# Optimization experiments

Measured on AMD Instinct MI355X. Metric: run time of the kernel, lower is better.

## Reference

```python
import jax, jax.numpy as jnp
import numpy as np

DILATIONS = [1, 2, 4]


def _lstm_cell(x, h, c, W_ih, W_hh, b_ih, b_hh):
    # PyTorch LSTMCell: gates in i, f, g, o order
    gates = x @ W_ih.T + b_ih + h @ W_hh.T + b_hh
    i, f, g, o = jnp.split(gates, 4, axis=-1)
    c_new = jax.nn.sigmoid(f) * c + jax.nn.sigmoid(i) * jnp.tanh(g)
    h_new = jax.nn.sigmoid(o) * jnp.tanh(c_new)
    return h_new, c_new


def _drnn_forward(x, params):
    B, T, _ = x.shape
    H = params[0][1].shape[1]
    L = len(params)
    # static per-(t, layer) update mask from dilations
    masks = jnp.asarray(
        np.array([[t % d == 0 for d in DILATIONS] for t in range(T)], dtype=bool)
    )  # [T, L]

    hs0 = tuple(jnp.zeros((B, H), x.dtype) for _ in range(L))
    cs0 = tuple(jnp.zeros((B, H), x.dtype) for _ in range(L))

    def step(carry, inp):
        hs, cs = carry
        x_t, m = inp  # x_t: [B, F], m: [L] bool
        hs = list(hs)
        cs = list(cs)
        for l, (Wi, Wh, bi, bh) in enumerate(params):
            inp_l = x_t if l == 0 else hs[l - 1]
            h_new, c_new = _lstm_cell(inp_l, hs[l], cs[l], Wi, Wh, bi, bh)
            hs[l] = jnp.where(m[l], h_new, hs[l])
            cs[l] = jnp.where(m[l], c_new, cs[l])
        return (tuple(hs), tuple(cs)), hs[-1]

    _, ys = jax.lax.scan(step, (hs0, cs0), (jnp.swapaxes(x, 0, 1), masks))
    return jnp.swapaxes(ys, 0, 1)  # [B, T, H]


def setup_inputs() -> dict:
    key = jax.random.key(0)
    ks = jax.random.split(key, 16)
    B, T, F, H = 128, 1024, 128, 256
    k = 1.0 / np.sqrt(H)  # torch LSTMCell init scale

    def u(kk, shape):
        return jax.random.uniform(kk, shape, jnp.float32, -k, k)

    inp = {"x": jax.random.normal(ks[0], (B, T, F), jnp.float32)}
    in_sizes = [F, H, H]
    ki = 1
    for l in range(3):
        inp[f"W_ih{l}"] = u(ks[ki], (4 * H, in_sizes[l])); ki += 1
        inp[f"W_hh{l}"] = u(ks[ki], (4 * H, H)); ki += 1
        inp[f"b_ih{l}"] = u(ks[ki], (4 * H,)); ki += 1
        inp[f"b_hh{l}"] = u(ks[ki], (4 * H,)); ki += 1
    return inp


def reference(x, W_ih0, W_hh0, b_ih0, b_hh0,
              W_ih1, W_hh1, b_ih1, b_hh1,
              W_ih2, W_hh2, b_ih2, b_hh2):
    params = [
        (W_ih0, W_hh0, b_ih0, b_hh0),
        (W_ih1, W_hh1, b_ih1, b_hh1),
        (W_ih2, W_hh2, b_ih2, b_hh2),
    ]
    return _drnn_forward(x, params)
```

## Files before the change

### kernel.cpp

```cpp
#include <hip/hip_runtime.h>
#include <hip/hip_fp16.h>
#include <stdint.h>
#include <stddef.h>


typedef _Float16 f16;
typedef _Float16 v2h __attribute__((ext_vector_type(2)));
typedef _Float16 v8h __attribute__((ext_vector_type(8)));
typedef __fp16 h2_raw __attribute__((ext_vector_type(2)));
typedef __fp16 h8_raw __attribute__((ext_vector_type(8)));
typedef float v4f __attribute__((ext_vector_type(4)));
typedef unsigned long long u64;

#define DEVINL static __device__ __forceinline__

DEVINL float sigm(float x) { return 1.0f / (1.0f + __expf(-x)); }
DEVINL float tanh_(float x) {
  x = fminf(fmaxf(x, -15.0f), 15.0f);
  float e = __expf(-2.0f * x);
  return (1.0f - e) / (1.0f + e);
}
DEVINL v2h pack2(float a, float b) {
  return __builtin_bit_cast(v2h, __builtin_amdgcn_cvt_pkrtz(a, b));
}
DEVINL v4f mfma_16x16x32(v8h a, v8h b, v4f c) {
  return __builtin_amdgcn_mfma_f32_16x16x32_f16(__builtin_bit_cast(h8_raw, a),
                                                __builtin_bit_cast(h8_raw, b), c,
                                                0, 0, 0);
}


__global__ void k_cvt_x(const float2* __restrict__ src, v2h* __restrict__ dst, int n2) {
  int i = blockIdx.x * blockDim.x + threadIdx.x;
  int st = gridDim.x * blockDim.x;
  for (; i < n2; i += st) {
    float2 v = src[i];
    dst[i] = pack2(v.x, v.y);
  }
}

__global__ void k_prep_w(const float* __restrict__ wih0, const float* __restrict__ whh0,
                         const float* __restrict__ wih1, const float* __restrict__ whh1,
                         const float* __restrict__ wih2, const float* __restrict__ whh2,
                         const float* __restrict__ bi0, const float* __restrict__ bh0,
                         const float* __restrict__ bi1, const float* __restrict__ bh1,
                         const float* __restrict__ bi2, const float* __restrict__ bh2,
                         f16* wih0f, f16* whh0f, f16* wih1f, f16* whh1f,
                         f16* wih2f, f16* whh2f,
                         float* bias0, float* bias1, float* bias2) {
  int i = blockIdx.x * blockDim.x + threadIdx.x;
  if (i < 131072) wih0f[i] = (f16)wih0[i];
  whh0f[i] = (f16)whh0[i];
  wih1f[i] = (f16)wih1[i];
  whh1f[i] = (f16)whh1[i];
  wih2f[i] = (f16)wih2[i];
  whh2f[i] = (f16)whh2[i];
  if (i < 1024) {
    bias0[i] = bi0[i] + bh0[i];
    bias1[i] = bi1[i] + bh1[i];
    bias2[i] = bi2[i] + bh2[i];
  }
}


template <int K>
__launch_bounds__(256)
__global__ void k_gemm(const f16* __restrict__ A, int Tb, int t0,
                       const f16* __restrict__ W, const float* __restrict__ bias,
                       f16* __restrict__ G) {
  constexpr int LDK = K + 8;
  __shared__ f16 As[64 * LDK];
  int b = blockIdx.x >> 2, tb = blockIdx.x & 3;
  const f16* Ablk = A + ((size_t)b * Tb + t0 + tb * 64) * K;
  int tid = threadIdx.x;

  constexpr int NV = 64 * K / 8;
  const uint4* src = (const uint4*)Ablk;
  for (int i = tid; i < NV; i += 256) {
    int e = i * 8;
    int r = e / K, c0 = e % K;
    *(uint4*)&As[r * LDK + c0] = src[i];
  }
  __syncthreads();

  int wave = tid >> 6, lane = tid & 63;
  int lm = lane & 15, lk = (lane >> 4) * 8;

  v8h af[K / 32];
#pragma unroll
  for (int kc = 0; kc < K / 32; ++kc)
    af[kc] = *(const v8h*)&As[(wave * 16 + lm) * LDK + kc * 32 + lk];

  size_t grow0 = (size_t)b * 256 + tb * 64 + wave * 16;
  for (int nt = 0; nt < 64; ++nt) {
    v4f acc = {0.0f, 0.0f, 0.0f, 0.0f};
    const f16* Wrow = W + (size_t)(nt * 16 + lm) * K + lk;
#pragma unroll
    for (int kc = 0; kc < K / 32; ++kc) {
      v8h bf = *(const v8h*)(Wrow + kc * 32);
      acc = mfma_16x16x32(af[kc], bf, acc);
    }
    float bv = bias[nt * 16 + lm];
#pragma unroll
    for (int r = 0; r < 4; ++r) {
      int m = (lane >> 4) * 4 + r;
      G[(grow0 + m) * 1024 + nt * 16 + lm] = (f16)(acc[r] + bv);
    }
  }
}


template <int LAYER>
__launch_bounds__(512, 2)
__global__ void k_rec(const f16* __restrict__ G,
                      const f16* __restrict__ Whh,
                      int t0, int steps,
                      f16* __restrict__ Hout, float* __restrict__ y,
                      float* __restrict__ hstate, float* __restrict__ cstate,
                      u64* hxw) {
  int blk = blockIdx.x;
  int g = blk & 15, half = blk >> 4;
  int tid = threadIdx.x;
  int lane = tid & 63;
  int wv = tid >> 6;

  int q = wv & 3, cs = wv >> 2;
  int colbase = q * 256 + half * 128 + cs * 64;
  int arow = lane & 15;
  int kq = (lane >> 4) * 8;

  int bl = wv, p = lane;
  int b = g * 8 + bl;

  __shared__ __align__(16) f16 hbuf[16][264];
  __shared__ float gq[4][8][132];

  v8h wf[32];
#pragma unroll
  for (int nt = 0; nt < 4; ++nt)
#pragma unroll
    for (int kt = 0; kt < 8; ++kt)
      wf[nt * 8 + kt] =
          *(const v8h*)&Whh[(size_t)(colbase + nt * 16 + arow) * 256 + kt * 32 + kq];

  {
    uint32_t* hz = (uint32_t*)&hbuf[0][0];
    for (int i = tid; i < 16 * 264 / 2; i += 512) hz[i] = 0u;
  }
  __syncthreads();

  float c0 = 0.0f, c1 = 0.0f, h0f = 0.0f, h1f = 0.0f;
  if (t0 > 0) {
    for (int w = tid; w < 1024; w += 512) {
      int rb = w >> 7, kp = w & 127;
      float2 hv = *(const float2*)&hstate[(size_t)(g * 8 + rb) * 256 + 2 * kp];
      *(uint32_t*)&hbuf[rb][2 * kp] = __builtin_bit_cast(uint32_t, pack2(hv.x, hv.y));
    }
    float2 cv = *(const float2*)&cstate[(size_t)b * 256 + half * 128 + 2 * p];
    c0 = cv.x;
    c1 = cv.y;
  }
  __syncthreads();

  u64* myw = hxw + (size_t)(g * 2 + half) * 1024;
  const u64* pw = hxw + (size_t)(g * 2 + (1 - half)) * 1024;

  const f16* Gc = G + (size_t)b * 256 * 1024 + half * 128 + 2 * p;
  uint32_t gv[4], gn[4];
#pragma unroll
  for (int j = 0; j < 4; ++j) gv[j] = *(const uint32_t*)&Gc[j * 256];

  for (int s = 0; s < steps; ++s) {
    int t = t0 + s;
    int par = t & 1;

    v4f acc[4] = {};
#pragma unroll
    for (int kt = 0; kt < 8; ++kt) {
      v8h a = *(const v8h*)&hbuf[arow][kt * 32 + kq];
#pragma unroll
      for (int nt = 0; nt < 4; ++nt)
        acc[nt] = mfma_16x16x32(a, wf[nt * 8 + kt], acc[nt]);
    }
    if (lane < 32) {
      int r0 = (lane >> 4) * 4;
      int d0 = cs * 64 + (lane & 15);
#pragma unroll
      for (int nt = 0; nt < 4; ++nt)
#pragma unroll
        for (int r = 0; r < 4; ++r)
          gq[q][r0 + r][d0 + nt * 16] = acc[nt][r];
    }
    if (s + 1 < steps) {
#pragma unroll
      for (int j = 0; j < 4; ++j)
        gn[j] = *(const uint32_t*)&Gc[(size_t)(s + 1) * 1024 + j * 256];
    }
    __syncthreads();

    const u64* pwp = &pw[(size_t)par * 512 + bl * 64 + p];
    u64 wp = __hip_atomic_load(pwp, __ATOMIC_RELAXED, __HIP_MEMORY_SCOPE_AGENT);

    float2 zi = *(const float2*)&gq[0][bl][2 * p];
    float2 zf = *(const float2*)&gq[1][bl][2 * p];
    float2 zg = *(const float2*)&gq[2][bl][2 * p];
    float2 zo = *(const float2*)&gq[3][bl][2 * p];
    v2h G0 = __builtin_bit_cast(v2h, gv[0]);
    v2h G1 = __builtin_bit_cast(v2h, gv[1]);
    v2h G2 = __builtin_bit_cast(v2h, gv[2]);
    v2h G3 = __builtin_bit_cast(v2h, gv[3]);

    float i0 = sigm(zi.x + (float)G0[0]), i1 = sigm(zi.y + (float)G0[1]);
    float f0 = sigm(zf.x + (float)G1[0]), f1 = sigm(zf.y + (float)G1[1]);
    float g0 = tanh_(zg.x + (float)G2[0]), g1 = tanh_(zg.y + (float)G2[1]);
    float o0 = sigm(zo.x + (float)G3[0]), o1 = sigm(zo.y + (float)G3[1]);
    c0 = f0 * c0 + i0 * g0;
    c1 = f1 * c1 + i1 * g1;
    h0f = o0 * tanh_(c0);
    h1f = o1 * tanh_(c1);

    uint32_t hp = __builtin_bit_cast(uint32_t, pack2(h0f, h1f));
    u64 word = ((u64)(uint32_t)(t + 1) << 32) | (u64)hp;
    __hip_atomic_store(&myw[(size_t)par * 512 + bl * 64 + p], word,
                       __ATOMIC_RELAXED, __HIP_MEMORY_SCOPE_AGENT);
    *(uint32_t*)&hbuf[bl][half * 128 + 2 * p] = hp;

    if (LAYER == 0) {
      if ((t & 1) == 0) {
        v2h hr; hr[0] = (f16)h0f; hr[1] = (f16)h1f;
        *(uint32_t*)&Hout[((size_t)b * 512 + (t >> 1)) * 256 + half * 128 + 2 * p] =
            __builtin_bit_cast(uint32_t, hr);
      }
    } else if (LAYER == 1) {
      if ((t & 1) == 0) {
        v2h hr; hr[0] = (f16)h0f; hr[1] = (f16)h1f;
        *(uint32_t*)&Hout[((size_t)b * 256 + (t >> 1)) * 256 + half * 128 + 2 * p] =
            __builtin_bit_cast(uint32_t, hr);
      }
    } else {
      size_t base = ((size_t)b * 1024 + (size_t)t * 4) * 256 + half * 128 + 2 * p;
      float2 hv; hv.x = h0f; hv.y = h1f;
      *(float2*)&y[base] = hv;
      *(float2*)&y[base + 256] = hv;
      *(float2*)&y[base + 512] = hv;
      *(float2*)&y[base + 768] = hv;
    }

    if (s + 1 < steps) {
      while ((int)(wp >> 32) < t + 1)
        wp = __hip_atomic_load(pwp, __ATOMIC_RELAXED, __HIP_MEMORY_SCOPE_AGENT);
      *(uint32_t*)&hbuf[bl][(1 - half) * 128 + 2 * p] = (uint32_t)wp;
    }
    __syncthreads();

#pragma unroll
    for (int j = 0; j < 4; ++j) gv[j] = gn[j];
  }

  size_t sb = (size_t)b * 256 + half * 128 + 2 * p;
  float2 hv; hv.x = h0f; hv.y = h1f;
  float2 cv; cv.x = c0; cv.y = c1;
  *(float2*)&hstate[sb] = hv;
  *(float2*)&cstate[sb] = cv;
}


extern "C" void kernel_launch(void* const* d_in, const int* in_sizes, int n_in,
                              void* d_out, int out_size, void* d_ws, size_t ws_size,
                              hipStream_t stream) {
  const float* x = (const float*)d_in[0];
  const float* wih[3] = {(const float*)d_in[1], (const float*)d_in[5], (const float*)d_in[9]};
  const float* whh[3] = {(const float*)d_in[2], (const float*)d_in[6], (const float*)d_in[10]};
  const float* bi[3] = {(const float*)d_in[3], (const float*)d_in[7], (const float*)d_in[11]};
  const float* bh[3] = {(const float*)d_in[4], (const float*)d_in[8], (const float*)d_in[12]};
  float* y = (float*)d_out;

  char* p = (char*)d_ws;
  f16* Xf = (f16*)p;        p += (size_t)16777216 * 2;
  f16* Wih0f = (f16*)p;     p += (size_t)131072 * 2;
  f16* Whh0f = (f16*)p;     p += (size_t)262144 * 2;
  f16* Wih1f = (f16*)p;     p += (size_t)262144 * 2;
  f16* Whh1f = (f16*)p;     p += (size_t)262144 * 2;
  f16* Wih2f = (f16*)p;     p += (size_t)262144 * 2;
  f16* Whh2f = (f16*)p;     p += (size_t)262144 * 2;
  float* bias0 = (float*)p; p += 4096;
  float* bias1 = (float*)p; p += 4096;
  float* bias2 = (float*)p; p += 4096;
  f16* Gbuf = (f16*)p;      p += (size_t)32768 * 1024 * 2;
  f16* H0e = (f16*)p;       p += (size_t)128 * 512 * 256 * 2;
  f16* H1q = (f16*)p;       p += (size_t)128 * 256 * 256 * 2;
  float* hstate = (float*)p; p += (size_t)128 * 256 * 4;
  float* cstate = (float*)p; p += (size_t)128 * 256 * 4;
  u64* hxw0 = (u64*)p;      p += (size_t)16 * 2 * 1024 * 8;
  u64* hxw1 = (u64*)p;      p += (size_t)16 * 2 * 1024 * 8;
  u64* hxw2 = (u64*)p;      p += (size_t)16 * 2 * 1024 * 8;

  k_cvt_x<<<4096, 256, 0, stream>>>((const float2*)x, (v2h*)Xf, 8388608);
  k_prep_w<<<1024, 256, 0, stream>>>(wih[0], whh[0], wih[1], whh[1], wih[2], whh[2],
                                     bi[0], bh[0], bi[1], bh[1], bi[2], bh[2],
                                     Wih0f, Whh0f, Wih1f, Whh1f, Wih2f, Whh2f,
                                     bias0, bias1, bias2);

  for (int c = 0; c < 4; ++c) {
    k_gemm<128><<<512, 256, 0, stream>>>(Xf, 1024, c * 256, Wih0f, bias0, Gbuf);
    k_rec<0><<<32, 512, 0, stream>>>(Gbuf, Whh0f, c * 256, 256, H0e, nullptr,
                                     hstate, cstate, hxw0);
  }
  for (int c = 0; c < 2; ++c) {
    k_gemm<256><<<512, 256, 0, stream>>>(H0e, 512, c * 256, Wih1f, bias1, Gbuf);
    k_rec<1><<<32, 512, 0, stream>>>(Gbuf, Whh1f, c * 256, 256, H1q, nullptr,
                                     hstate, cstate, hxw1);
  }
  k_gemm<256><<<512, 256, 0, stream>>>(H1q, 256, 0, Wih2f, bias2, Gbuf);
  k_rec<2><<<32, 512, 0, stream>>>(Gbuf, Whh2f, 0, 256, nullptr, y,
                                   hstate, cstate, hxw2);
}
```

Measured before the change: 4.501 ms.

## Process two batch groups per recurrent block with swizzled LDS and lighter barriers

Each recurrent block now handles two independent 8-row batch groups, and the grid shrinks from 32 to 16 blocks. Each block interleaves two MFMA/cell pipelines so one group's cross-block handshake latency can be hidden behind the other's work, reusing the register-resident Whh fragments. The h buffer drops row padding in favour of an XOR-swizzled layout to avoid LDS bank conflicts. __syncthreads is replaced with a custom barrier that waits only on lgkmcnt. The risk is about twice the serial work per block per step, and fewer CUs in use.

```diff
diff --git a/kernel.cpp b/kernel.cpp
--- a/kernel.cpp
+++ b/kernel.cpp
@@ -27,6 +27,23 @@
   return __builtin_amdgcn_mfma_f32_16x16x32_f16(__builtin_bit_cast(h8_raw, a),
                                                 __builtin_bit_cast(h8_raw, b), c,
                                                 0, 0, 0);
+}
+
+DEVINL void wg_barrier() {
+  __builtin_amdgcn_sched_barrier(0);
+  asm volatile("s_waitcnt lgkmcnt(0)" ::: "memory");
+  __builtin_amdgcn_s_barrier();
+  asm volatile("" ::: "memory");
+  __builtin_amdgcn_sched_barrier(0);
+}
+
+DEVINL uint32_t* hb_word(f16 (*hb)[256], int row, int wd) {
+  int ch = (wd >> 2) ^ (row & 7);
+  return (uint32_t*)((char*)hb + row * 512 + ch * 16 + (wd & 3) * 4);
+}
+DEVINL v8h hb_frag(const f16 (*hb)[256], int row, int kt, int s4) {
+  int ch = (kt * 4 + s4) ^ (row & 7);
+  return *(const v8h*)((const char*)hb + row * 512 + ch * 16);
 }
 
 
@@ -110,6 +127,26 @@
 }
 
 
+#define LSTM_CELL(gq, gv, c0v, c1v, h0v, h1v)                                 \
+  {                                                                           \
+    float2 zi = *(const float2*)&gq[0][bl][2 * p];                            \
+    float2 zf = *(const float2*)&gq[1][bl][2 * p];                            \
+    float2 zg = *(const float2*)&gq[2][bl][2 * p];                            \
+    float2 zo = *(const float2*)&gq[3][bl][2 * p];                            \
+    v2h G0 = __builtin_bit_cast(v2h, gv[0]);                                  \
+    v2h G1 = __builtin_bit_cast(v2h, gv[1]);                                  \
+    v2h G2 = __builtin_bit_cast(v2h, gv[2]);                                  \
+    v2h G3 = __builtin_bit_cast(v2h, gv[3]);                                  \
+    float i0 = sigm(zi.x + (float)G0[0]), i1 = sigm(zi.y + (float)G0[1]);     \
+    float f0 = sigm(zf.x + (float)G1[0]), f1 = sigm(zf.y + (float)G1[1]);     \
+    float g0v = tanh_(zg.x + (float)G2[0]), g1v = tanh_(zg.y + (float)G2[1]); \
+    float o0 = sigm(zo.x + (float)G3[0]), o1 = sigm(zo.y + (float)G3[1]);     \
+    c0v = f0 * c0v + i0 * g0v;                                                \
+    c1v = f1 * c1v + i1 * g1v;                                                \
+    h0v = o0 * tanh_(c0v);                                                    \
+    h1v = o1 * tanh_(c1v);                                                    \
+  }
+
 template <int LAYER>
 __launch_bounds__(512, 2)
 __global__ void k_rec(const f16* __restrict__ G,
@@ -119,21 +156,21 @@
                       float* __restrict__ hstate, float* __restrict__ cstate,
                       u64* hxw) {
   int blk = blockIdx.x;
-  int g = blk & 15, half = blk >> 4;
+  int pr = blk & 7, half = blk >> 3;
+  int g0 = pr * 2, g1 = pr * 2 + 1;
   int tid = threadIdx.x;
   int lane = tid & 63;
   int wv = tid >> 6;
 
   int q = wv & 3, cs = wv >> 2;
   int colbase = q * 256 + half * 128 + cs * 64;
-  int arow = lane & 15;
-  int kq = (lane >> 4) * 8;
+  int arow = lane & 15, s4 = lane >> 4, kq = s4 * 8;
 
   int bl = wv, p = lane;
-  int b = g * 8 + bl;
-
-  __shared__ __align__(16) f16 hbuf[16][264];
-  __shared__ float gq[4][8][132];
+  int bA = g0 * 8 + bl, bB = g1 * 8 + bl;
+
+  __shared__ __align__(16) f16 hbA[16][256], hbB[16][256];
+  __shared__ float gqA[4][8][132], gqB[4][8][132];
 
   v8h wf[32];
 #pragma unroll
@@ -142,126 +179,179 @@
     for (int kt = 0; kt < 8; ++kt)
       wf[nt * 8 + kt] =
           *(const v8h*)&Whh[(size_t)(colbase + nt * 16 + arow) * 256 + kt * 32 + kq];
+#pragma unroll
+  for (int i = 0; i < 32; ++i)
+    asm volatile("" : "+v"(wf[i]));
 
   {
-    uint32_t* hz = (uint32_t*)&hbuf[0][0];
-    for (int i = tid; i < 16 * 264 / 2; i += 512) hz[i] = 0u;
+    uint32_t* z0 = (uint32_t*)&hbA[0][0];
+    uint32_t* z1 = (uint32_t*)&hbB[0][0];
+    for (int i = tid; i < 2048; i += 512) { z0[i] = 0u; z1[i] = 0u; }
   }
   __syncthreads();
 
-  float c0 = 0.0f, c1 = 0.0f, h0f = 0.0f, h1f = 0.0f;
+  float cA0 = 0.f, cA1 = 0.f, hA0 = 0.f, hA1 = 0.f;
+  float cB0 = 0.f, cB1 = 0.f, hB0 = 0.f, hB1 = 0.f;
   if (t0 > 0) {
     for (int w = tid; w < 1024; w += 512) {
       int rb = w >> 7, kp = w & 127;
-      float2 hv = *(const float2*)&hstate[(size_t)(g * 8 + rb) * 256 + 2 * kp];
-      *(uint32_t*)&hbuf[rb][2 * kp] = __builtin_bit_cast(uint32_t, pack2(hv.x, hv.y));
-    }
-    float2 cv = *(const float2*)&cstate[(size_t)b * 256 + half * 128 + 2 * p];
-    c0 = cv.x;
-    c1 = cv.y;
+      float2 ha = *(const float2*)&hstate[(size_t)(g0 * 8 + rb) * 256 + 2 * kp];
+      *hb_word(hbA, rb, kp) = __builtin_bit_cast(uint32_t, pack2(ha.x, ha.y));
+      float2 hb = *(const float2*)&hstate[(size_t)(g1 * 8 + rb) * 256 + 2 * kp];
+      *hb_word(hbB, rb, kp) = __builtin_bit_cast(uint32_t, pack2(hb.x, hb.y));
+    }
+    float2 ca = *(const float2*)&cstate[(size_t)bA * 256 + half * 128 + 2 * p];
+    cA0 = ca.x; cA1 = ca.y;
+    float2 cb = *(const float2*)&cstate[(size_t)bB * 256 + half * 128 + 2 * p];
+    cB0 = cb.x; cB1 = cb.y;
   }
   __syncthreads();
 
-  u64* myw = hxw + (size_t)(g * 2 + half) * 1024;
-  const u64* pw = hxw + (size_t)(g * 2 + (1 - half)) * 1024;
-
-  const f16* Gc = G + (size_t)b * 256 * 1024 + half * 128 + 2 * p;
-  uint32_t gv[4], gn[4];
-#pragma unroll
-  for (int j = 0; j < 4; ++j) gv[j] = *(const uint32_t*)&Gc[j * 256];
+  u64* pubA = hxw + (size_t)(g0 * 2 + half) * 1024;
+  const u64* pwA = hxw + (size_t)(g0 * 2 + (1 - half)) * 1024;
+  u64* pubB = hxw + (size_t)(g1 * 2 + half) * 1024;
+  const u64* pwB = hxw + (size_t)(g1 * 2 + (1 - half)) * 1024;
+
+  const f16* GcA = G + (size_t)bA * 256 * 1024 + half * 128 + 2 * p;
+  const f16* GcB = G + (size_t)bB * 256 * 1024 + half * 128 + 2 * p;
+  uint32_t gvA[4], gvB[4], gnA[4], gnB[4];
+#pragma unroll
+  for (int j = 0; j < 4; ++j) {
+    gvA[j] = *(const uint32_t*)&GcA[j * 256];
+    gvB[j] = *(const uint32_t*)&GcB[j * 256];
+  }
 
   for (int s = 0; s < steps; ++s) {
     int t = t0 + s;
     int par = t & 1;
 
-    v4f acc[4] = {};
-#pragma unroll
-    for (int kt = 0; kt < 8; ++kt) {
-      v8h a = *(const v8h*)&hbuf[arow][kt * 32 + kq];
-#pragma unroll
-      for (int nt = 0; nt < 4; ++nt)
-        acc[nt] = mfma_16x16x32(a, wf[nt * 8 + kt], acc[nt]);
-    }
-    if (lane < 32) {
-      int r0 = (lane >> 4) * 4;
-      int d0 = cs * 64 + (lane & 15);
-#pragma unroll
-      for (int nt = 0; nt < 4; ++nt)
-#pragma unroll
-        for (int r = 0; r < 4; ++r)
-          gq[q][r0 + r][d0 + nt * 16] = acc[nt][r];
+    {
+      v4f acc[4] = {{0.f, 0.f, 0.f, 0.f}, {0.f, 0.f, 0.f, 0.f},
+                    {0.f, 0.f, 0.f, 0.f}, {0.f, 0.f, 0.f, 0.f}};
+#pragma unroll
+      for (int kt = 0; kt < 8; ++kt) {
+        v8h a = hb_frag(hbA, arow, kt, s4);
+#pragma unroll
+        for (int nt = 0; nt < 4; ++nt)
+          acc[nt] = mfma_16x16x32(a, wf[nt * 8 + kt], acc[nt]);
+      }
+      if (lane < 32) {
+        int r0 = (lane >> 4) * 4, d0 = cs * 64 + (lane & 15);
+#pragma unroll
+        for (int nt = 0; nt < 4; ++nt)
+#pragma unroll
+          for (int r = 0; r < 4; ++r)
+            gqA[q][r0 + r][d0 + nt * 16] = acc[nt][r];
+      }
+    }
+    {
+      v4f acc[4] = {{0.f, 0.f, 0.f, 0.f}, {0.f, 0.f, 0.f, 0.f},
+                    {0.f, 0.f, 0.f, 0.f}, {0.f, 0.f, 0.f, 0.f}};
+#pragma unroll
+      for (int kt = 0; kt < 8; ++kt) {
+        v8h a = hb_frag(hbB, arow, kt, s4);
+#pragma unroll
+        for (int nt = 0; nt < 4; ++nt)
+          acc[nt] = mfma_16x16x32(a, wf[nt * 8 + kt], acc[nt]);
+      }
+      if (lane < 32) {
+        int r0 = (lane >> 4) * 4, d0 = cs * 64 + (lane & 15);
+#pragma unroll
+        for (int nt = 0; nt < 4; ++nt)
+#pragma unroll
+          for (int r = 0; r < 4; ++r)
+            gqB[q][r0 + r][d0 + nt * 16] = acc[nt][r];
+      }
     }
     if (s + 1 < steps) {
 #pragma unroll
-      for (int j = 0; j < 4; ++j)
-        gn[j] = *(const uint32_t*)&Gc[(size_t)(s + 1) * 1024 + j * 256];
-    }
-    __syncthreads();
-
-    const u64* pwp = &pw[(size_t)par * 512 + bl * 64 + p];
-    u64 wp = __hip_atomic_load(pwp, __ATOMIC_RELAXED, __HIP_MEMORY_SCOPE_AGENT);
-
-    float2 zi = *(const float2*)&gq[0][bl][2 * p];
-    float2 zf = *(const float2*)&gq[1][bl][2 * p];
-    float2 zg = *(const float2*)&gq[2][bl][2 * p];
-    float2 zo = *(const float2*)&gq[3][bl][2 * p];
-    v2h G0 = __builtin_bit_cast(v2h, gv[0]);
-    v2h G1 = __builtin_bit_cast(v2h, gv[1]);
-    v2h G2 = __builtin_bit_cast(v2h, gv[2]);
-    v2h G3 = __builtin_bit_cast(v2h, gv[3]);
-
-    float i0 = sigm(zi.x + (float)G0[0]), i1 = sigm(zi.y + (float)G0[1]);
-    float f0 = sigm(zf.x + (float)G1[0]), f1 = sigm(zf.y + (float)G1[1]);
-    float g0 = tanh_(zg.x + (float)G2[0]), g1 = tanh_(zg.y + (float)G2[1]);
-    float o0 = sigm(zo.x + (float)G3[0]), o1 = sigm(zo.y + (float)G3[1]);
-    c0 = f0 * c0 + i0 * g0;
-    c1 = f1 * c1 + i1 * g1;
-    h0f = o0 * tanh_(c0);
-    h1f = o1 * tanh_(c1);
-
-    uint32_t hp = __builtin_bit_cast(uint32_t, pack2(h0f, h1f));
-    u64 word = ((u64)(uint32_t)(t + 1) << 32) | (u64)hp;
-    __hip_atomic_store(&myw[(size_t)par * 512 + bl * 64 + p], word,
+      for (int j = 0; j < 4; ++j) {
+        gnA[j] = *(const uint32_t*)&GcA[(size_t)(s + 1) * 1024 + j * 256];
+        gnB[j] = *(const uint32_t*)&GcB[(size_t)(s + 1) * 1024 + j * 256];
+      }
+    }
+    wg_barrier();
+
+    const u64* ppA = &pwA[(size_t)par * 512 + bl * 64 + p];
+    const u64* ppB = &pwB[(size_t)par * 512 + bl * 64 + p];
+    u64 wpA = __hip_atomic_load(ppA, __ATOMIC_RELAXED, __HIP_MEMORY_SCOPE_AGENT);
+    u64 wpB = __hip_atomic_load(ppB, __ATOMIC_RELAXED, __HIP_MEMORY_SCOPE_AGENT);
+
+    LSTM_CELL(gqA, gvA, cA0, cA1, hA0, hA1);
+    uint32_t hpA = __builtin_bit_cast(uint32_t, pack2(hA0, hA1));
+    __hip_atomic_store(&pubA[(size_t)par * 512 + bl * 64 + p],
+                       ((u64)(uint32_t)(t + 1) << 32) | (u64)hpA,
                        __ATOMIC_RELAXED, __HIP_MEMORY_SCOPE_AGENT);
-    *(uint32_t*)&hbuf[bl][half * 128 + 2 * p] = hp;
+    *hb_word(hbA, bl, half * 64 + p) = hpA;
+
+    LSTM_CELL(gqB, gvB, cB0, cB1, hB0, hB1);
+    uint32_t hpB = __builtin_bit_cast(uint32_t, pack2(hB0, hB1));
+    __hip_atomic_store(&pubB[(size_t)par * 512 + bl * 64 + p],
+                       ((u64)(uint32_t)(t + 1) << 32) | (u64)hpB,
+                       __ATOMIC_RELAXED, __HIP_MEMORY_SCOPE_AGENT);
+    *hb_word(hbB, bl, half * 64 + p) = hpB;
 
     if (LAYER == 0) {
       if ((t & 1) == 0) {
-        v2h hr; hr[0] = (f16)h0f; hr[1] = (f16)h1f;
-        *(uint32_t*)&Hout[((size_t)b * 512 + (t >> 1)) * 256 + half * 128 + 2 * p] =
+        v2h hr;
+        hr[0] = (f16)hA0; hr[1] = (f16)hA1;
+        *(uint32_t*)&Hout[((size_t)bA * 512 + (t >> 1)) * 256 + half * 128 + 2 * p] =
+            __builtin_bit_cast(uint32_t, hr);
+        hr[0] = (f16)hB0; hr[1] = (f16)hB1;
+        *(uint32_t*)&Hout[((size_t)bB * 512 + (t >> 1)) * 256 + half * 128 + 2 * p] =
             __builtin_bit_cast(uint32_t, hr);
       }
     } else if (LAYER == 1) {
       if ((t & 1) == 0) {
-        v2h hr; hr[0] = (f16)h0f; hr[1] = (f16)h1f;
-        *(uint32_t*)&Hout[((size_t)b * 256 + (t >> 1)) * 256 + half * 128 + 2 * p] =
+        v2h hr;
+        hr[0] = (f16)hA0; hr[1] = (f16)hA1;
+        *(uint32_t*)&Hout[((size_t)bA * 256 + (t >> 1)) * 256 + half * 128 + 2 * p] =
             __builtin_bit_cast(uint32_t, hr);
+        hr[0] = (f16)hB0; hr[1] = (f16)hB1;
+        *(uint32_t*)&Hout[((size_t)bB * 256 + (t >> 1)) * 256 + half * 128 + 2 * p] =
+            __builtin_bit_cast(uint32_t, hr);
       }
     } else {
-      size_t base = ((size_t)b * 1024 + (size_t)t * 4) * 256 + half * 128 + 2 * p;
-      float2 hv; hv.x = h0f; hv.y = h1f;
-      *(float2*)&y[base] = hv;
-      *(float2*)&y[base + 256] = hv;
-      *(float2*)&y[base + 512] = hv;
-      *(float2*)&y[base + 768] = hv;
+      size_t baseA = ((size_t)bA * 1024 + (size_t)t * 4) * 256 + half * 128 + 2 * p;
+      float2 hvA; hvA.x = hA0; hvA.y = hA1;
+      *(float2*)&y[baseA] = hvA;
+      *(float2*)&y[baseA + 256] = hvA;
+      *(float2*)&y[baseA + 512] = hvA;
+      *(float2*)&y[baseA + 768] = hvA;
+      size_t baseB = ((size_t)bB * 1024 + (size_t)t * 4) * 256 + half * 128 + 2 * p;
+      float2 hvB; hvB.x = hB0; hvB.y = hB1;
+      *(float2*)&y[baseB] = hvB;
+      *(float2*)&y[baseB + 256] = hvB;
+      *(float2*)&y[baseB + 512] = hvB;
+      *(float2*)&y[baseB + 768] = hvB;
     }
 
     if (s + 1 < steps) {
-      while ((int)(wp >> 32) < t + 1)
-        wp = __hip_atomic_load(pwp, __ATOMIC_RELAXED, __HIP_MEMORY_SCOPE_AGENT);
-      *(uint32_t*)&hbuf[bl][(1 - half) * 128 + 2 * p] = (uint32_t)wp;
-    }
-    __syncthreads();
-
-#pragma unroll
-    for (int j = 0; j < 4; ++j) gv[j] = gn[j];
-  }
-
-  size_t sb = (size_t)b * 256 + half * 128 + 2 * p;
-  float2 hv; hv.x = h0f; hv.y = h1f;
-  float2 cv; cv.x = c0; cv.y = c1;
-  *(float2*)&hstate[sb] = hv;
-  *(float2*)&cstate[sb] = cv;
+      while ((int)(wpA >> 32) < t + 1)
+        wpA = __hip_atomic_load(ppA, __ATOMIC_RELAXED, __HIP_MEMORY_SCOPE_AGENT);
+      *hb_word(hbA, bl, (1 - half) * 64 + p) = (uint32_t)wpA;
+      while ((int)(wpB >> 32) < t + 1)
+        wpB = __hip_atomic_load(ppB, __ATOMIC_RELAXED, __HIP_MEMORY_SCOPE_AGENT);
+      *hb_word(hbB, bl, (1 - half) * 64 + p) = (uint32_t)wpB;
+    }
+    wg_barrier();
+
+#pragma unroll
+    for (int j = 0; j < 4; ++j) { gvA[j] = gnA[j]; gvB[j] = gnB[j]; }
+  }
+
+  {
+    size_t sbA = (size_t)bA * 256 + half * 128 + 2 * p;
+    float2 hv; hv.x = hA0; hv.y = hA1;
+    float2 cv; cv.x = cA0; cv.y = cA1;
+    *(float2*)&hstate[sbA] = hv;
+    *(float2*)&cstate[sbA] = cv;
+    size_t sbB = (size_t)bB * 256 + half * 128 + 2 * p;
+    float2 hw; hw.x = hB0; hw.y = hB1;
+    float2 cw; cw.x = cB0; cw.y = cB1;
+    *(float2*)&hstate[sbB] = hw;
+    *(float2*)&cstate[sbB] = cw;
+  }
 }
 
 
@@ -303,15 +393,15 @@
 
   for (int c = 0; c < 4; ++c) {
     k_gemm<128><<<512, 256, 0, stream>>>(Xf, 1024, c * 256, Wih0f, bias0, Gbuf);
-    k_rec<0><<<32, 512, 0, stream>>>(Gbuf, Whh0f, c * 256, 256, H0e, nullptr,
+    k_rec<0><<<16, 512, 0, stream>>>(Gbuf, Whh0f, c * 256, 256, H0e, nullptr,
                                      hstate, cstate, hxw0);
   }
   for (int c = 0; c < 2; ++c) {
     k_gemm<256><<<512, 256, 0, stream>>>(H0e, 512, c * 256, Wih1f, bias1, Gbuf);
-    k_rec<1><<<32, 512, 0, stream>>>(Gbuf, Whh1f, c * 256, 256, H1q, nullptr,
+    k_rec<1><<<16, 512, 0, stream>>>(Gbuf, Whh1f, c * 256, 256, H1q, nullptr,
                                      hstate, cstate, hxw1);
   }
   k_gemm<256><<<512, 256, 0, stream>>>(H1q, 256, 0, Wih2f, bias2, Gbuf);
-  k_rec<2><<<32, 512, 0, stream>>>(Gbuf, Whh2f, 0, 256, nullptr, y,
+  k_rec<2><<<16, 512, 0, stream>>>(Gbuf, Whh2f, 0, 256, nullptr, y,
                                    hstate, cstate, hxw2);
 }
```

After: 7.143 ms. 58.7% more time.

## Split recurrent LSTM across 16 column blocks per batch group with wider exchange

Applied to the files above, without the earlier changes.

Each group of 8 batch rows now uses 16 workgroups instead of 2, each owning a 16-column slice of hidden units. The W_hh fragment per wave shrinks to 8 registers. Every step, each workgroup gathers the full hidden vector from all peers through a flag-stamped global exchange buffer, and hbuf is XOR-swizzled to avoid LDS bank conflicts. The intent is to shorten the serial per-step MFMA chain and spread work over more CUs, at the cost of many more cross-workgroup polls and global traffic per timestep, with only 16 of 64 lanes doing cell math.

```diff
diff --git a/kernel.cpp b/kernel.cpp
--- a/kernel.cpp
+++ b/kernel.cpp
@@ -27,6 +27,14 @@
   return __builtin_amdgcn_mfma_f32_16x16x32_f16(__builtin_bit_cast(h8_raw, a),
                                                 __builtin_bit_cast(h8_raw, b), c,
                                                 0, 0, 0);
+}
+
+DEVINL void wg_barrier() {
+  __builtin_amdgcn_sched_barrier(0);
+  asm volatile("s_waitcnt lgkmcnt(0)" ::: "memory");
+  __builtin_amdgcn_s_barrier();
+  asm volatile("" ::: "memory");
+  __builtin_amdgcn_sched_barrier(0);
 }
 
 
@@ -111,7 +119,7 @@
 
 
 template <int LAYER>
-__launch_bounds__(512, 2)
+__launch_bounds__(256)
 __global__ void k_rec(const f16* __restrict__ G,
                       const f16* __restrict__ Whh,
                       int t0, int steps,
@@ -119,149 +127,176 @@
                       float* __restrict__ hstate, float* __restrict__ cstate,
                       u64* hxw) {
   int blk = blockIdx.x;
-  int g = blk & 15, half = blk >> 4;
+  int g = blk & 15, sub = blk >> 4;
+  int d0 = sub * 16;
   int tid = threadIdx.x;
-  int lane = tid & 63;
-  int wv = tid >> 6;
-
-  int q = wv & 3, cs = wv >> 2;
-  int colbase = q * 256 + half * 128 + cs * 64;
-  int arow = lane & 15;
-  int kq = (lane >> 4) * 8;
-
-  int bl = wv, p = lane;
+  int lane = tid & 63, wv = tid >> 6;
+  int q = wv;
+  int arow = lane & 15, s4 = lane >> 4;
+
+  bool is_cell = (lane < 16);
+  int bl = 2 * wv + (lane >> 3);
+  int wp = lane & 7;
   int b = g * 8 + bl;
 
-  __shared__ __align__(16) f16 hbuf[16][264];
-  __shared__ float gq[4][8][132];
-
-  v8h wf[32];
-#pragma unroll
-  for (int nt = 0; nt < 4; ++nt)
-#pragma unroll
-    for (int kt = 0; kt < 8; ++kt)
-      wf[nt * 8 + kt] =
-          *(const v8h*)&Whh[(size_t)(colbase + nt * 16 + arow) * 256 + kt * 32 + kq];
-
+  int pbl = tid >> 5;
+  int pwd = (tid & 31) * 4;
+
+  __shared__ __align__(16) f16 hbuf[16][256];
+  __shared__ float gq[4][8][18];
+
+  v8h wf[8];
   {
-    uint32_t* hz = (uint32_t*)&hbuf[0][0];
-    for (int i = tid; i < 16 * 264 / 2; i += 512) hz[i] = 0u;
+    const v8h* wrow = (const v8h*)&Whh[(size_t)(q * 256 + d0 + arow) * 256];
+#pragma unroll
+    for (int kt = 0; kt < 8; ++kt) wf[kt] = wrow[kt * 4 + s4];
+#pragma unroll
+    for (int i = 0; i < 8; ++i)
+      asm volatile("" : "+v"(wf[i]));
+  }
+
+  char* fillp = (char*)hbuf + pbl * 512 + (((tid & 31) ^ (pbl & 7)) * 16);
+  char* fillz = (char*)hbuf + (8 + pbl) * 512 + (((tid & 31) ^ (pbl & 7)) * 16);
+
+  float c0 = 0.f, c1 = 0.f, h0 = 0.f, h1 = 0.f;
+  {
+    uint4 z = {0u, 0u, 0u, 0u};
+    *(uint4*)fillz = z;
+    if (t0 == 0) {
+      *(uint4*)fillp = z;
+    } else {
+      int bq = g * 8 + pbl;
+      const float4* hs = (const float4*)&hstate[(size_t)bq * 256 + 2 * pwd];
+      float4 u = hs[0], v = hs[1];
+      uint4 pk;
+      pk.x = __builtin_bit_cast(uint32_t, pack2(u.x, u.y));
+      pk.y = __builtin_bit_cast(uint32_t, pack2(u.z, u.w));
+      pk.z = __builtin_bit_cast(uint32_t, pack2(v.x, v.y));
+      pk.w = __builtin_bit_cast(uint32_t, pack2(v.z, v.w));
+      *(uint4*)fillp = pk;
+      if (is_cell) {
+        float2 cc = *(const float2*)&cstate[(size_t)b * 256 + d0 + 2 * wp];
+        c0 = cc.x; c1 = cc.y;
+      }
+    }
   }
   __syncthreads();
 
-  float c0 = 0.0f, c1 = 0.0f, h0f = 0.0f, h1f = 0.0f;
-  if (t0 > 0) {
-    for (int w = tid; w < 1024; w += 512) {
-      int rb = w >> 7, kp = w & 127;
-      float2 hv = *(const float2*)&hstate[(size_t)(g * 8 + rb) * 256 + 2 * kp];
-      *(uint32_t*)&hbuf[rb][2 * kp] = __builtin_bit_cast(uint32_t, pack2(hv.x, hv.y));
-    }
-    float2 cv = *(const float2*)&cstate[(size_t)b * 256 + half * 128 + 2 * p];
-    c0 = cv.x;
-    c1 = cv.y;
-  }
-  __syncthreads();
-
-  u64* myw = hxw + (size_t)(g * 2 + half) * 1024;
-  const u64* pw = hxw + (size_t)(g * 2 + (1 - half)) * 1024;
-
-  const f16* Gc = G + (size_t)b * 256 * 1024 + half * 128 + 2 * p;
-  uint32_t gv[4], gn[4];
-#pragma unroll
-  for (int j = 0; j < 4; ++j) gv[j] = *(const uint32_t*)&Gc[j * 256];
+  u64* hx_g = hxw + (size_t)g * 2048;
+  u64* pubp = hx_g + (size_t)bl * 128 + (d0 >> 1) + wp;
+  const u64* pollp = hx_g + (size_t)pbl * 128 + pwd;
+
+  const f16* Gc = G + (size_t)b * 262144 + d0 + 2 * wp;
+  uint32_t gv[4] = {0, 0, 0, 0}, gn[4] = {0, 0, 0, 0};
+  if (is_cell) {
+#pragma unroll
+    for (int j = 0; j < 4; ++j) gv[j] = *(const uint32_t*)&Gc[j * 256];
+  }
 
   for (int s = 0; s < steps; ++s) {
     int t = t0 + s;
-    int par = t & 1;
-
-    v4f acc[4] = {};
-#pragma unroll
-    for (int kt = 0; kt < 8; ++kt) {
-      v8h a = *(const v8h*)&hbuf[arow][kt * 32 + kq];
-#pragma unroll
-      for (int nt = 0; nt < 4; ++nt)
-        acc[nt] = mfma_16x16x32(a, wf[nt * 8 + kt], acc[nt]);
+    int pp = (t + 1) & 1;
+
+    v4f acc0 = {0.f, 0.f, 0.f, 0.f}, acc1 = {0.f, 0.f, 0.f, 0.f};
+#pragma unroll
+    for (int kt = 0; kt < 8; kt += 2) {
+      v8h a0 = *(const v8h*)((const char*)hbuf + arow * 512 +
+                             (((kt * 4 + s4) ^ (arow & 7)) * 16));
+      acc0 = mfma_16x16x32(a0, wf[kt], acc0);
+      v8h a1 = *(const v8h*)((const char*)hbuf + arow * 512 +
+                             ((((kt + 1) * 4 + s4) ^ (arow & 7)) * 16));
+      acc1 = mfma_16x16x32(a1, wf[kt + 1], acc1);
     }
     if (lane < 32) {
-      int r0 = (lane >> 4) * 4;
-      int d0 = cs * 64 + (lane & 15);
-#pragma unroll
-      for (int nt = 0; nt < 4; ++nt)
-#pragma unroll
-        for (int r = 0; r < 4; ++r)
-          gq[q][r0 + r][d0 + nt * 16] = acc[nt][r];
-    }
-    if (s + 1 < steps) {
+      int r0 = s4 * 4;
+#pragma unroll
+      for (int r = 0; r < 4; ++r) gq[q][r0 + r][arow] = acc0[r] + acc1[r];
+    }
+    if (is_cell && s + 1 < steps) {
 #pragma unroll
       for (int j = 0; j < 4; ++j)
         gn[j] = *(const uint32_t*)&Gc[(size_t)(s + 1) * 1024 + j * 256];
     }
-    __syncthreads();
-
-    const u64* pwp = &pw[(size_t)par * 512 + bl * 64 + p];
-    u64 wp = __hip_atomic_load(pwp, __ATOMIC_RELAXED, __HIP_MEMORY_SCOPE_AGENT);
-
-    float2 zi = *(const float2*)&gq[0][bl][2 * p];
-    float2 zf = *(const float2*)&gq[1][bl][2 * p];
-    float2 zg = *(const float2*)&gq[2][bl][2 * p];
-    float2 zo = *(const float2*)&gq[3][bl][2 * p];
-    v2h G0 = __builtin_bit_cast(v2h, gv[0]);
-    v2h G1 = __builtin_bit_cast(v2h, gv[1]);
-    v2h G2 = __builtin_bit_cast(v2h, gv[2]);
-    v2h G3 = __builtin_bit_cast(v2h, gv[3]);
-
-    float i0 = sigm(zi.x + (float)G0[0]), i1 = sigm(zi.y + (float)G0[1]);
-    float f0 = sigm(zf.x + (float)G1[0]), f1 = sigm(zf.y + (float)G1[1]);
-    float g0 = tanh_(zg.x + (float)G2[0]), g1 = tanh_(zg.y + (float)G2[1]);
-    float o0 = sigm(zo.x + (float)G3[0]), o1 = sigm(zo.y + (float)G3[1]);
-    c0 = f0 * c0 + i0 * g0;
-    c1 = f1 * c1 + i1 * g1;
-    h0f = o0 * tanh_(c0);
-    h1f = o1 * tanh_(c1);
-
-    uint32_t hp = __builtin_bit_cast(uint32_t, pack2(h0f, h1f));
-    u64 word = ((u64)(uint32_t)(t + 1) << 32) | (u64)hp;
-    __hip_atomic_store(&myw[(size_t)par * 512 + bl * 64 + p], word,
-                       __ATOMIC_RELAXED, __HIP_MEMORY_SCOPE_AGENT);
-    *(uint32_t*)&hbuf[bl][half * 128 + 2 * p] = hp;
-
-    if (LAYER == 0) {
-      if ((t & 1) == 0) {
-        v2h hr; hr[0] = (f16)h0f; hr[1] = (f16)h1f;
-        *(uint32_t*)&Hout[((size_t)b * 512 + (t >> 1)) * 256 + half * 128 + 2 * p] =
-            __builtin_bit_cast(uint32_t, hr);
+    wg_barrier();
+
+    if (is_cell) {
+      float2 zi = *(const float2*)&gq[0][bl][2 * wp];
+      float2 zf = *(const float2*)&gq[1][bl][2 * wp];
+      float2 zg = *(const float2*)&gq[2][bl][2 * wp];
+      float2 zo = *(const float2*)&gq[3][bl][2 * wp];
+      v2h G0 = __builtin_bit_cast(v2h, gv[0]);
+      v2h G1 = __builtin_bit_cast(v2h, gv[1]);
+      v2h G2 = __builtin_bit_cast(v2h, gv[2]);
+      v2h G3 = __builtin_bit_cast(v2h, gv[3]);
+      float i0 = sigm(zi.x + (float)G0[0]), i1 = sigm(zi.y + (float)G0[1]);
+      float f0 = sigm(zf.x + (float)G1[0]), f1 = sigm(zf.y + (float)G1[1]);
+      float g0 = tanh_(zg.x + (float)G2[0]), g1 = tanh_(zg.y + (float)G2[1]);
+      float o0 = sigm(zo.x + (float)G3[0]), o1 = sigm(zo.y + (float)G3[1]);
+      c0 = f0 * c0 + i0 * g0;
+      c1 = f1 * c1 + i1 * g1;
+      h0 = o0 * tanh_(c0);
+      h1 = o1 * tanh_(c1);
+
+      uint32_t hp = __builtin_bit_cast(uint32_t, pack2(h0, h1));
+      __hip_atomic_store(pubp + (size_t)pp * 1024,
+                         ((u64)(uint32_t)(t + 1) << 32) | (u64)hp,
+                         __ATOMIC_RELAXED, __HIP_MEMORY_SCOPE_AGENT);
+
+      if (LAYER == 0) {
+        if ((t & 1) == 0) {
+          v2h hr; hr[0] = (f16)h0; hr[1] = (f16)h1;
+          *(uint32_t*)&Hout[((size_t)b * 512 + (t >> 1)) * 256 + d0 + 2 * wp] =
+              __builtin_bit_cast(uint32_t, hr);
+        }
+      } else if (LAYER == 1) {
+        if ((t & 1) == 0) {
+          v2h hr; hr[0] = (f16)h0; hr[1] = (f16)h1;
+          *(uint32_t*)&Hout[((size_t)b * 256 + (t >> 1)) * 256 + d0 + 2 * wp] =
+              __builtin_bit_cast(uint32_t, hr);
+        }
+      } else {
+        size_t base = ((size_t)b * 1024 + (size_t)t * 4) * 256 + d0 + 2 * wp;
+        float2 hv; hv.x = h0; hv.y = h1;
+        *(float2*)&y[base] = hv;
+        *(float2*)&y[base + 256] = hv;
+        *(float2*)&y[base + 512] = hv;
+        *(float2*)&y[base + 768] = hv;
       }
-    } else if (LAYER == 1) {
-      if ((t & 1) == 0) {
-        v2h hr; hr[0] = (f16)h0f; hr[1] = (f16)h1f;
-        *(uint32_t*)&Hout[((size_t)b * 256 + (t >> 1)) * 256 + half * 128 + 2 * p] =
-            __builtin_bit_cast(uint32_t, hr);
+    }
+
+    if (s + 1 < steps) {
+      const u64* pb = pollp + (size_t)pp * 1024;
+      int tau = t + 1;
+      u64 w0, w1, w2, w3;
+      for (;;) {
+        w0 = __hip_atomic_load(pb + 0, __ATOMIC_RELAXED, __HIP_MEMORY_SCOPE_AGENT);
+        w1 = __hip_atomic_load(pb + 1, __ATOMIC_RELAXED, __HIP_MEMORY_SCOPE_AGENT);
+        w2 = __hip_atomic_load(pb + 2, __ATOMIC_RELAXED, __HIP_MEMORY_SCOPE_AGENT);
+        w3 = __hip_atomic_load(pb + 3, __ATOMIC_RELAXED, __HIP_MEMORY_SCOPE_AGENT);
+        if ((int)(w0 >> 32) >= tau && (int)(w1 >> 32) >= tau &&
+            (int)(w2 >> 32) >= tau && (int)(w3 >> 32) >= tau)
+          break;
       }
-    } else {
-      size_t base = ((size_t)b * 1024 + (size_t)t * 4) * 256 + half * 128 + 2 * p;
-      float2 hv; hv.x = h0f; hv.y = h1f;
-      *(float2*)&y[base] = hv;
-      *(float2*)&y[base + 256] = hv;
-      *(float2*)&y[base + 512] = hv;
-      *(float2*)&y[base + 768] = hv;
-    }
-
-    if (s + 1 < steps) {
-      while ((int)(wp >> 32) < t + 1)
-        wp = __hip_atomic_load(pwp, __ATOMIC_RELAXED, __HIP_MEMORY_SCOPE_AGENT);
-      *(uint32_t*)&hbuf[bl][(1 - half) * 128 + 2 * p] = (uint32_t)wp;
-    }
-    __syncthreads();
-
-#pragma unroll
-    for (int j = 0; j < 4; ++j) gv[j] = gn[j];
-  }
-
-  size_t sb = (size_t)b * 256 + half * 128 + 2 * p;
-  float2 hv; hv.x = h0f; hv.y = h1f;
-  float2 cv; cv.x = c0; cv.y = c1;
-  *(float2*)&hstate[sb] = hv;
-  *(float2*)&cstate[sb] = cv;
+      uint4 pk;
+      pk.x = (uint32_t)w0; pk.y = (uint32_t)w1;
+      pk.z = (uint32_t)w2; pk.w = (uint32_t)w3;
+      *(uint4*)fillp = pk;
+    }
+    wg_barrier();
+
+    if (is_cell) {
+#pragma unroll
+      for (int j = 0; j < 4; ++j) gv[j] = gn[j];
+    }
+  }
+
+  if (is_cell) {
+    size_t sb = (size_t)b * 256 + d0 + 2 * wp;
+    float2 hv; hv.x = h0; hv.y = h1;
+    float2 cv; cv.x = c0; cv.y = c1;
+    *(float2*)&hstate[sb] = hv;
+    *(float2*)&cstate[sb] = cv;
+  }
 }
 
 
@@ -303,15 +338,15 @@
 
   for (int c = 0; c < 4; ++c) {
     k_gemm<128><<<512, 256, 0, stream>>>(Xf, 1024, c * 256, Wih0f, bias0, Gbuf);
-    k_rec<0><<<32, 512, 0, stream>>>(Gbuf, Whh0f, c * 256, 256, H0e, nullptr,
-                                     hstate, cstate, hxw0);
+    k_rec<0><<<256, 256, 0, stream>>>(Gbuf, Whh0f, c * 256, 256, H0e, nullptr,
+                                      hstate, cstate, hxw0);
   }
   for (int c = 0; c < 2; ++c) {
     k_gemm<256><<<512, 256, 0, stream>>>(H0e, 512, c * 256, Wih1f, bias1, Gbuf);
-    k_rec<1><<<32, 512, 0, stream>>>(Gbuf, Whh1f, c * 256, 256, H1q, nullptr,
-                                     hstate, cstate, hxw1);
+    k_rec<1><<<256, 256, 0, stream>>>(Gbuf, Whh1f, c * 256, 256, H1q, nullptr,
+                                      hstate, cstate, hxw1);
   }
   k_gemm<256><<<512, 256, 0, stream>>>(H1q, 256, 0, Wih2f, bias2, Gbuf);
-  k_rec<2><<<32, 512, 0, stream>>>(Gbuf, Whh2f, 0, 256, nullptr, y,
-                                   hstate, cstate, hxw2);
-}
+  k_rec<2><<<256, 256, 0, stream>>>(Gbuf, Whh2f, 0, 256, nullptr, y,
+                                    hstate, cstate, hxw2);
+}
```

Measured after the change: 4.679 ms. 1.04x slower.
